# Kernel optimization log

Measured on AMD Instinct MI355X. Metric: run time of the kernel, lower is better.

The kernel has to match this reference:

```python
import jax, jax.numpy as jnp
import numpy as np

N_NODES = 100000
N_EDGES = 3200000
IN_SIZE, HIDDEN, OUT_SIZE = 512, 16, 64


def setup_inputs() -> dict:
    key = jax.random.key(0)
    k1, k2, k3, k4, k5, k6 = jax.random.split(key, 6)
    x = jax.random.normal(k1, (N_NODES, IN_SIZE), dtype=jnp.float32)
    src = jax.random.randint(k2, (N_EDGES,), 0, N_NODES, dtype=jnp.int64)
    dst = jax.random.randint(k3, (N_EDGES,), 0, N_NODES, dtype=jnp.int64)
    # Glorot-style init like dgl GraphConv
    W1 = jax.random.normal(k4, (IN_SIZE, HIDDEN), dtype=jnp.float32) * (1.0 / np.sqrt(IN_SIZE))
    b1 = jnp.zeros((HIDDEN,), dtype=jnp.float32)
    W2 = jax.random.normal(k5, (HIDDEN, OUT_SIZE), dtype=jnp.float32) * (1.0 / np.sqrt(HIDDEN))
    b2 = jnp.zeros((OUT_SIZE,), dtype=jnp.float32)
    return {"x": x, "W1": W1, "b1": b1, "W2": W2, "b2": b2, "src": src, "dst": dst}


def _degree_norms(src, dst, n_nodes):
    ones = jnp.ones(src.shape[0], dtype=jnp.float32)
    deg_out = jnp.clip(jax.ops.segment_sum(ones, src, num_segments=n_nodes), 1.0)
    deg_in = jnp.clip(jax.ops.segment_sum(ones, dst, num_segments=n_nodes), 1.0)
    return deg_out ** -0.5, deg_in ** -0.5  # norm='both' as in dgl GraphConv


def _graph_conv(x, W, b, src, dst, norm_src, norm_dst, transform_first):
    # dgl GraphConv: applies W before aggregation when in_feats > out_feats
    h = x * norm_src[:, None]
    if transform_first:
        h = h @ W
    # SpMM: gather from src, scatter-sum to dst
    agg = jax.ops.segment_sum(h[src], dst, num_segments=x.shape[0])
    if not transform_first:
        agg = agg @ W
    return agg * norm_dst[:, None] + b


def reference(x, W1, b1, W2, b2, src, dst):
    n = x.shape[0]
    norm_src, norm_dst = _degree_norms(src, dst, n)
    h = _graph_conv(x, W1, b1, src, dst, norm_src, norm_dst, transform_first=True)  # 512>16
    h = jax.nn.relu(h)
    out = _graph_conv(h, W2, b2, src, dst, norm_src, norm_dst, transform_first=False)  # 16<64
    return out
```

## Files before the change

kernel.cpp:

```cpp
#include <hip/hip_runtime.h>

#define NT 256
#define NBC 49
#define CAPC 69632
#define EPBC 8192
#define CAP 16384
#define MAXF 512

typedef __bf16 bf16x8 __attribute__((ext_vector_type(8)));
typedef float f32x4 __attribute__((ext_vector_type(4)));

__device__ __forceinline__ unsigned short f2bf(float f) {
    unsigned int u = __float_as_uint(f);
    unsigned int r = u + 0x7FFFu + ((u >> 16) & 1u);
    return (unsigned short)(r >> 16);
}
__device__ __forceinline__ float bf2f(unsigned short h) {
    return __uint_as_float(((unsigned int)h) << 16);
}

__global__ __launch_bounds__(512) void init_all(int* __restrict__ gcurCD,
                                                int* __restrict__ gcurCS,
                                                int* __restrict__ gcurF,
                                                const float* __restrict__ W1,
                                                unsigned short* __restrict__ w1t_hi,
                                                unsigned short* __restrict__ w1t_lo, int nbf) {
    if (blockIdx.x == 0) {
        int i = threadIdx.x;
        if (i < NBC) { gcurCD[i] = i * CAPC; gcurCS[i] = i * CAPC; }
        if (i < nbf) gcurF[i] = i * CAP;
    } else {
        int t = (blockIdx.x - 1) * 512 + threadIdx.x;
        if (t < 512 * 16) {
            int k = t >> 4, c = t & 15;
            float f = W1[k * 16 + c];
            unsigned short h = f2bf(f);
            w1t_hi[c * 512 + k] = h;
            w1t_lo[c * 512 + k] = f2bf(f - bf2f(h));
        }
    }
}

__global__ __launch_bounds__(NT) void coarse_scatter(const int* __restrict__ src,
                                                     const int* __restrict__ dst,
                                                     int* __restrict__ gcurCD,
                                                     int* __restrict__ gcurCS,
                                                     unsigned int* __restrict__ ebinCD,
                                                     unsigned short* __restrict__ ebinCS,
                                                     int e) {
    __shared__ int hD[NBC], hS[NBC], cD[NBC], cS[NBC];
    int tid = threadIdx.x;
    if (tid < NBC) { hD[tid] = 0; hS[tid] = 0; }
    __syncthreads();
    int p0 = blockIdx.x * EPBC;
    int pend = min(p0 + EPBC, e);
    for (int p = p0 + tid; p < pend; p += NT) {
        atomicAdd(&hD[dst[p] >> 11], 1);
        atomicAdd(&hS[src[p] >> 11], 1);
    }
    __syncthreads();
    if (tid < NBC) {
        cD[tid] = hD[tid] ? atomicAdd(&gcurCD[tid], hD[tid]) : 0;
        cS[tid] = hS[tid] ? atomicAdd(&gcurCS[tid], hS[tid]) : 0;
    }
    __syncthreads();
    for (int p = p0 + tid; p < pend; p += NT) {
        int s = src[p], d = dst[p];
        int c = d >> 11;
        int slot = atomicAdd(&cD[c], 1);
        if (slot < (c + 1) * CAPC)
            ebinCD[slot] = (unsigned int)s | ((unsigned int)(d & 2047) << 17);
        int cs = s >> 11;
        int slot2 = atomicAdd(&cS[cs], 1);
        if (slot2 < (cs + 1) * CAPC)
            ebinCS[slot2] = (unsigned short)(s & 2047);
    }
}

__global__ __launch_bounds__(NT) void fine_scatter(const unsigned int* __restrict__ ebinCD,
                                                   const int* __restrict__ gcurCD,
                                                   int* __restrict__ gcurF,
                                                   unsigned int* __restrict__ ebinD) {
    __shared__ int hF[8], cF[8];
    int c = blockIdx.x >> 3, k = blockIdx.x & 7;
    int tid = threadIdx.x;
    if (tid < 8) hF[tid] = 0;
    __syncthreads();
    int p0c = c * CAPC;
    int p1 = gcurCD[c];
    int len = p1 - p0c;
    int chunk = (len + 7) >> 3;
    int q0 = p0c + k * chunk;
    int q1 = min(q0 + chunk, p1);
    for (int p = q0 + tid; p < q1; p += NT)
        atomicAdd(&hF[(ebinCD[p] >> 25) & 7], 1);
    __syncthreads();
    if (tid < 8) {
        int h = hF[tid];
        cF[tid] = h ? atomicAdd(&gcurF[c * 8 + tid], h) : 0;
    }
    __syncthreads();
    for (int p = q0 + tid; p < q1; p += NT) {
        unsigned int w = ebinCD[p];
        int f = (w >> 25) & 7;
        int slot = atomicAdd(&cF[f], 1);
        if (slot < (c * 8 + f + 1) * CAP)
            ebinD[slot] = (w & 0x1FFFFu) | (((w >> 17) & 255u) << 17);
    }
}

__global__ __launch_bounds__(NT) void s_hist(const unsigned short* __restrict__ ebinCS,
                                             const int* __restrict__ gcurCS,
                                             int* __restrict__ cntS, int n) {
    __shared__ int cnt[2048];
    int c = blockIdx.x >> 3, k = blockIdx.x & 7;
    int tid = threadIdx.x;
    for (int i = tid; i < 2048; i += NT) cnt[i] = 0;
    __syncthreads();
    int p0c = c * CAPC;
    int p1 = gcurCS[c];
    int len = p1 - p0c;
    int chunk = (len + 7) >> 3;
    int q0 = p0c + k * chunk;
    int q1 = min(q0 + chunk, p1);
    for (int p = q0 + tid; p < q1; p += NT)
        atomicAdd(&cnt[ebinCS[p]], 1);
    __syncthreads();
    int node0 = c * 2048;
    for (int i = tid; i < 2048; i += NT) {
        int v = cnt[i];
        if (v && node0 + i < n) atomicAdd(&cntS[node0 + i], v);
    }
}

#define GR 64
__global__ __launch_bounds__(NT) void gemm1_mfma(const float* __restrict__ x,
                                                 const unsigned short* __restrict__ w1t_hi,
                                                 const unsigned short* __restrict__ w1t_lo,
                                                 const int* __restrict__ cntS,
                                                 unsigned short* __restrict__ y1bf, int n) {
    __shared__ __attribute__((aligned(16))) unsigned short sh_hi[GR][72];
    __shared__ __attribute__((aligned(16))) unsigned short sh_lo[GR][72];
    int tid = threadIdx.x;
    int w = tid >> 6, l = tid & 63;
    int row0 = blockIdx.x * GR;

    f32x4 acc = {0.f, 0.f, 0.f, 0.f};
    int col = l & 15;
    int kq = (l >> 4) * 8;
    int arow = w * 16 + (l & 15);

    for (int kc = 0; kc < 512; kc += 64) {
        __syncthreads();
#pragma unroll
        for (int i = 0; i < 4; i++) {
            int idx = tid + i * NT;
            int r = idx >> 4;
            int c4 = idx & 15;
            int grow = row0 + r;
            float4 v = make_float4(0.f, 0.f, 0.f, 0.f);
            if (grow < n) v = *(const float4*)&x[(size_t)grow * 512 + kc + c4 * 4];
            ushort4 hv, lv;
            hv.x = f2bf(v.x); lv.x = f2bf(v.x - bf2f(hv.x));
            hv.y = f2bf(v.y); lv.y = f2bf(v.y - bf2f(hv.y));
            hv.z = f2bf(v.z); lv.z = f2bf(v.z - bf2f(hv.z));
            hv.w = f2bf(v.w); lv.w = f2bf(v.w - bf2f(hv.w));
            *(ushort4*)&sh_hi[r][c4 * 4] = hv;
            *(ushort4*)&sh_lo[r][c4 * 4] = lv;
        }
        __syncthreads();
#pragma unroll
        for (int ks = 0; ks < 2; ks++) {
            int klocal = ks * 32 + kq;
            bf16x8 a_hi = *(const bf16x8*)&sh_hi[arow][klocal];
            bf16x8 a_lo = *(const bf16x8*)&sh_lo[arow][klocal];
            int kglob = kc + klocal;
            bf16x8 b_hi = *(const bf16x8*)&w1t_hi[col * 512 + kglob];
            bf16x8 b_lo = *(const bf16x8*)&w1t_lo[col * 512 + kglob];
            acc = __builtin_amdgcn_mfma_f32_16x16x32_bf16(a_hi, b_hi, acc, 0, 0, 0);
            acc = __builtin_amdgcn_mfma_f32_16x16x32_bf16(a_lo, b_hi, acc, 0, 0, 0);
            acc = __builtin_amdgcn_mfma_f32_16x16x32_bf16(a_hi, b_lo, acc, 0, 0, 0);
        }
    }

    int rbase = (l >> 4) * 4;
#pragma unroll
    for (int reg = 0; reg < 4; reg++) {
        int grow = row0 + w * 16 + rbase + reg;
        if (grow < n) {
            float ns = rsqrtf((float)max(cntS[grow], 1));
            y1bf[(size_t)grow * 16 + col] = f2bf(acc[reg] * ns);
        }
    }
}

__global__ __launch_bounds__(NT) void dst_fill(const unsigned int* __restrict__ ebinD,
                                               const int* __restrict__ gcurF,
                                               int* __restrict__ rowoff,
                                               int* __restrict__ rowend,
                                               float* __restrict__ norm_dst,
                                               int* __restrict__ esrc, int n) {
    __shared__ int cnt[256], cur[256], tmp[256];
    int b = blockIdx.x, tid = threadIdx.x;
    cnt[tid] = 0;
    __syncthreads();
    int p0 = b * CAP, p1 = gcurF[b];
    for (int p = p0 + tid; p < p1; p += NT) atomicAdd(&cnt[ebinD[p] >> 17], 1);
    __syncthreads();
    int v = cnt[tid];
    int val = v;
    tmp[tid] = val;
    __syncthreads();
    for (int off = 1; off < 256; off <<= 1) {
        int a = (tid >= off) ? tmp[tid - off] : 0;
        __syncthreads();
        val += a;
        tmp[tid] = val;
        __syncthreads();
    }
    int excl = val - v;
    int node = (b << 8) + tid;
    if (node < n) {
        rowoff[node] = p0 + excl;
        rowend[node] = p0 + excl + v;
        norm_dst[node] = rsqrtf((float)max(v, 1));
    }
    cur[tid] = p0 + excl;
    __syncthreads();
    for (int p = p0 + tid; p < p1; p += NT) {
        unsigned int w = ebinD[p];
        int pos = atomicAdd(&cur[w >> 17], 1);
        esrc[pos] = (int)(w & 0x1FFFFu);
    }
}

__global__ __launch_bounds__(NT) void aggregate_act(const unsigned short* __restrict__ feat,
                                                    const int* __restrict__ rowoff,
                                                    const int* __restrict__ rowend,
                                                    const int* __restrict__ esrc,
                                                    const float* __restrict__ norm_dst,
                                                    const int* __restrict__ cntS,
                                                    const float* __restrict__ b1,
                                                    unsigned short* __restrict__ h1s, int n) {
    int tid = threadIdx.x;
    int d = blockIdx.x * 16 + (tid >> 4);
    int j = tid & 15;
    if (d >= n) return;
    int p = rowoff[d], end = rowend[d];
    float a0 = 0.f, a1 = 0.f, a2 = 0.f, a3 = 0.f;
    for (; p + 3 < end; p += 4) {
        int s0 = esrc[p], s1 = esrc[p + 1], s2 = esrc[p + 2], s3 = esrc[p + 3];
        a0 += bf2f(feat[(size_t)s0 * 16 + j]);
        a1 += bf2f(feat[(size_t)s1 * 16 + j]);
        a2 += bf2f(feat[(size_t)s2 * 16 + j]);
        a3 += bf2f(feat[(size_t)s3 * 16 + j]);
    }
    for (; p < end; ++p) a0 += bf2f(feat[(size_t)esrc[p] * 16 + j]);
    float acc = (a0 + a1) + (a2 + a3);
    float ns = rsqrtf((float)max(cntS[d], 1));
    float v = fmaxf(acc * norm_dst[d] + b1[j], 0.f) * ns;
    h1s[(size_t)d * 16 + j] = f2bf(v);
}

__global__ __launch_bounds__(NT) void aggregate_final(const unsigned short* __restrict__ feat,
                                                      const int* __restrict__ rowoff,
                                                      const int* __restrict__ rowend,
                                                      const int* __restrict__ esrc,
                                                      const float* __restrict__ norm_dst,
                                                      const float* __restrict__ W2,
                                                      const float* __restrict__ b2,
                                                      float* __restrict__ out, int n) {
    __shared__ float sW[16 * 64];
    int tid = threadIdx.x;
    *(float4*)&sW[tid * 4] = *(const float4*)&W2[tid * 4];
    __syncthreads();
    int d = blockIdx.x * 16 + (tid >> 4);
    int j = tid & 15;
    if (d >= n) return;
    int p = rowoff[d], end = rowend[d];
    float a0 = 0.f, a1 = 0.f, a2 = 0.f, a3 = 0.f;
    for (; p + 3 < end; p += 4) {
        int s0 = esrc[p], s1 = esrc[p + 1], s2 = esrc[p + 2], s3 = esrc[p + 3];
        a0 += bf2f(feat[(size_t)s0 * 16 + j]);
        a1 += bf2f(feat[(size_t)s1 * 16 + j]);
        a2 += bf2f(feat[(size_t)s2 * 16 + j]);
        a3 += bf2f(feat[(size_t)s3 * 16 + j]);
    }
    for (; p < end; ++p) a0 += bf2f(feat[(size_t)esrc[p] * 16 + j]);
    float acc = (a0 + a1) + (a2 + a3);
    float nd = norm_dst[d];
    float o0 = 0.f, o1 = 0.f, o2 = 0.f, o3 = 0.f;
#pragma unroll
    for (int k = 0; k < 16; k++) {
        float ak = __shfl(acc, k, 16);
        o0 += ak * sW[k * 64 + j];
        o1 += ak * sW[k * 64 + j + 16];
        o2 += ak * sW[k * 64 + j + 32];
        o3 += ak * sW[k * 64 + j + 48];
    }
    size_t ob = (size_t)d * 64;
    out[ob + j]      = o0 * nd + b2[j];
    out[ob + j + 16] = o1 * nd + b2[j + 16];
    out[ob + j + 32] = o2 * nd + b2[j + 32];
    out[ob + j + 48] = o3 * nd + b2[j + 48];
}

extern "C" void kernel_launch(void* const* d_in, const int* in_sizes, int n_in,
                              void* d_out, int out_size, void* d_ws, size_t ws_size,
                              hipStream_t stream) {
    const float* x  = (const float*)d_in[0];
    const float* W1 = (const float*)d_in[1];
    const float* b1 = (const float*)d_in[2];
    const float* W2 = (const float*)d_in[3];
    const float* b2 = (const float*)d_in[4];
    const int* src  = (const int*)d_in[5];
    const int* dst  = (const int*)d_in[6];

    int n = in_sizes[0] / 512;
    int e = in_sizes[5];
    float* out = (float*)d_out;

    int nbf = (n + 255) >> 8;

    char* ws = (char*)d_ws;
    size_t off = 0;
    auto alloc = [&](size_t bytes) { size_t o = off; off = (off + bytes + 255) & ~(size_t)255; return o; };
    int*   cntS   = (int*)(ws + alloc((size_t)n * 4));
    size_t zero_end = off;
    int*   gcurCD = (int*)(ws + alloc(NBC * 4));
    int*   gcurCS = (int*)(ws + alloc(NBC * 4));
    int*   gcurF  = (int*)(ws + alloc(MAXF * 4));
    float* norm_dst = (float*)(ws + alloc((size_t)n * 4));
    int*   rowoff   = (int*)(ws + alloc((size_t)n * 4));
    int*   rowend   = (int*)(ws + alloc((size_t)n * 4));
    unsigned int*   ebinCD = (unsigned int*)(ws + alloc((size_t)NBC * CAPC * 4));
    unsigned short* ebinCS = (unsigned short*)(ws + alloc((size_t)NBC * CAPC * 2));
    unsigned int*   ebinD  = (unsigned int*)(ws + alloc((size_t)nbf * CAP * 4));
    int*   esrc  = (int*)(ws + alloc((size_t)nbf * CAP * 4));
    unsigned short* y1bf = (unsigned short*)(ws + alloc((size_t)n * 16 * 2));
    unsigned short* h1s  = (unsigned short*)(ws + alloc((size_t)n * 16 * 2));
    unsigned short* w1t_hi = (unsigned short*)(ws + alloc(16 * 512 * 2));
    unsigned short* w1t_lo = (unsigned short*)(ws + alloc(16 * 512 * 2));
    if (off > ws_size) return;

    int cbb = (e + EPBC - 1) / EPBC;
    int fbb = NBC * 8;
    int grb = (n + GR - 1) / GR;
    int agb = (n + 15) / 16;

    hipMemsetAsync(cntS, 0, zero_end, stream);

    init_all       <<<17, 512, 0, stream>>>(gcurCD, gcurCS, gcurF, W1, w1t_hi, w1t_lo, nbf);
    coarse_scatter <<<cbb, NT, 0, stream>>>(src, dst, gcurCD, gcurCS, ebinCD, ebinCS, e);
    fine_scatter   <<<fbb, NT, 0, stream>>>(ebinCD, gcurCD, gcurF, ebinD);
    s_hist         <<<fbb, NT, 0, stream>>>(ebinCS, gcurCS, cntS, n);
    gemm1_mfma     <<<grb, NT, 0, stream>>>(x, w1t_hi, w1t_lo, cntS, y1bf, n);
    dst_fill       <<<nbf, NT, 0, stream>>>(ebinD, gcurF, rowoff, rowend, norm_dst, esrc, n);
    aggregate_act  <<<agb, NT, 0, stream>>>(y1bf, rowoff, rowend, esrc, norm_dst, cntS, b1, h1s, n);
    aggregate_final<<<agb, NT, 0, stream>>>(h1s, rowoff, rowend, esrc, norm_dst, W2, b2, out, n);
}
```

Baseline: 245.0 us.

## Merge fine scatter with source histogram and use one wavefront per node in aggregation

Merges the fine_scatter and s_hist kernels into one launch whose blocks branch on block index, so the two independent passes run side by side and one launch is saved. The two aggregation kernels now give each destination node a full 64-lane wavefront instead of 16 lanes. Within a node, four lane groups walk the neighbour list in parallel, two edges per group per step, and the partial sums are combined with cross-lane shuffles. This exposes more memory-level parallelism on the irregular gathers. In exchange, many lanes sit idle on low-degree nodes, and there are four times as many blocks.

```diff
diff --git a/kernel.cpp b/kernel.cpp
--- a/kernel.cpp
+++ b/kernel.cpp
@@ -77,59 +77,60 @@
     }
 }
 
-__global__ __launch_bounds__(NT) void fine_scatter(const unsigned int* __restrict__ ebinCD,
-                                                   const int* __restrict__ gcurCD,
-                                                   int* __restrict__ gcurF,
-                                                   unsigned int* __restrict__ ebinD) {
-    __shared__ int hF[8], cF[8];
-    int c = blockIdx.x >> 3, k = blockIdx.x & 7;
+__global__ __launch_bounds__(NT) void fine_plus_shist(const unsigned int* __restrict__ ebinCD,
+                                                      const int* __restrict__ gcurCD,
+                                                      int* __restrict__ gcurF,
+                                                      unsigned int* __restrict__ ebinD,
+                                                      const unsigned short* __restrict__ ebinCS,
+                                                      const int* __restrict__ gcurCS,
+                                                      int* __restrict__ cntS, int n) {
     int tid = threadIdx.x;
-    if (tid < 8) hF[tid] = 0;
-    __syncthreads();
-    int p0c = c * CAPC;
-    int p1 = gcurCD[c];
-    int len = p1 - p0c;
-    int chunk = (len + 7) >> 3;
-    int q0 = p0c + k * chunk;
-    int q1 = min(q0 + chunk, p1);
-    for (int p = q0 + tid; p < q1; p += NT)
-        atomicAdd(&hF[(ebinCD[p] >> 25) & 7], 1);
-    __syncthreads();
-    if (tid < 8) {
-        int h = hF[tid];
-        cF[tid] = h ? atomicAdd(&gcurF[c * 8 + tid], h) : 0;
-    }
-    __syncthreads();
-    for (int p = q0 + tid; p < q1; p += NT) {
-        unsigned int w = ebinCD[p];
-        int f = (w >> 25) & 7;
-        int slot = atomicAdd(&cF[f], 1);
-        if (slot < (c * 8 + f + 1) * CAP)
-            ebinD[slot] = (w & 0x1FFFFu) | (((w >> 17) & 255u) << 17);
-    }
-}
-
-__global__ __launch_bounds__(NT) void s_hist(const unsigned short* __restrict__ ebinCS,
-                                             const int* __restrict__ gcurCS,
-                                             int* __restrict__ cntS, int n) {
-    __shared__ int cnt[2048];
-    int c = blockIdx.x >> 3, k = blockIdx.x & 7;
-    int tid = threadIdx.x;
-    for (int i = tid; i < 2048; i += NT) cnt[i] = 0;
-    __syncthreads();
-    int p0c = c * CAPC;
-    int p1 = gcurCS[c];
-    int len = p1 - p0c;
-    int chunk = (len + 7) >> 3;
-    int q0 = p0c + k * chunk;
-    int q1 = min(q0 + chunk, p1);
-    for (int p = q0 + tid; p < q1; p += NT)
-        atomicAdd(&cnt[ebinCS[p]], 1);
-    __syncthreads();
-    int node0 = c * 2048;
-    for (int i = tid; i < 2048; i += NT) {
-        int v = cnt[i];
-        if (v && node0 + i < n) atomicAdd(&cntS[node0 + i], v);
+    if (blockIdx.x < NBC * 8) {
+        __shared__ int hF[8], cF[8];
+        int c = blockIdx.x >> 3, k = blockIdx.x & 7;
+        if (tid < 8) hF[tid] = 0;
+        __syncthreads();
+        int p0c = c * CAPC;
+        int p1 = gcurCD[c];
+        int len = p1 - p0c;
+        int chunk = (len + 7) >> 3;
+        int q0 = p0c + k * chunk;
+        int q1 = min(q0 + chunk, p1);
+        for (int p = q0 + tid; p < q1; p += NT)
+            atomicAdd(&hF[(ebinCD[p] >> 25) & 7], 1);
+        __syncthreads();
+        if (tid < 8) {
+            int h = hF[tid];
+            cF[tid] = h ? atomicAdd(&gcurF[c * 8 + tid], h) : 0;
+        }
+        __syncthreads();
+        for (int p = q0 + tid; p < q1; p += NT) {
+            unsigned int w = ebinCD[p];
+            int f = (w >> 25) & 7;
+            int slot = atomicAdd(&cF[f], 1);
+            if (slot < (c * 8 + f + 1) * CAP)
+                ebinD[slot] = (w & 0x1FFFFu) | (((w >> 17) & 255u) << 17);
+        }
+    } else {
+        __shared__ int cnt[2048];
+        int bb = blockIdx.x - NBC * 8;
+        int c = bb >> 3, k = bb & 7;
+        for (int i = tid; i < 2048; i += NT) cnt[i] = 0;
+        __syncthreads();
+        int p0c = c * CAPC;
+        int p1 = gcurCS[c];
+        int len = p1 - p0c;
+        int chunk = (len + 7) >> 3;
+        int q0 = p0c + k * chunk;
+        int q1 = min(q0 + chunk, p1);
+        for (int p = q0 + tid; p < q1; p += NT)
+            atomicAdd(&cnt[ebinCS[p]], 1);
+        __syncthreads();
+        int node0 = c * 2048;
+        for (int i = tid; i < 2048; i += NT) {
+            int v = cnt[i];
+            if (v && node0 + i < n) atomicAdd(&cntS[node0 + i], v);
+        }
     }
 }
 
@@ -242,24 +243,26 @@
                                                     const int* __restrict__ cntS,
                                                     const float* __restrict__ b1,
                                                     unsigned short* __restrict__ h1s, int n) {
-    int tid = threadIdx.x;
-    int d = blockIdx.x * 16 + (tid >> 4);
-    int j = tid & 15;
+    int d = blockIdx.x * 4 + (threadIdx.x >> 6);
     if (d >= n) return;
-    int p = rowoff[d], end = rowend[d];
-    float a0 = 0.f, a1 = 0.f, a2 = 0.f, a3 = 0.f;
-    for (; p + 3 < end; p += 4) {
-        int s0 = esrc[p], s1 = esrc[p + 1], s2 = esrc[p + 2], s3 = esrc[p + 3];
-        a0 += bf2f(feat[(size_t)s0 * 16 + j]);
-        a1 += bf2f(feat[(size_t)s1 * 16 + j]);
-        a2 += bf2f(feat[(size_t)s2 * 16 + j]);
-        a3 += bf2f(feat[(size_t)s3 * 16 + j]);
-    }
-    for (; p < end; ++p) a0 += bf2f(feat[(size_t)esrc[p] * 16 + j]);
-    float acc = (a0 + a1) + (a2 + a3);
-    float ns = rsqrtf((float)max(cntS[d], 1));
-    float v = fmaxf(acc * norm_dst[d] + b1[j], 0.f) * ns;
-    h1s[(size_t)d * 16 + j] = f2bf(v);
+    int l = threadIdx.x & 63;
+    int g = l >> 4, j = l & 15;
+    int p0 = rowoff[d], p1 = rowend[d];
+    float acc = 0.f;
+    for (int p = p0; p < p1; p += 8) {
+        int pe0 = p + g, pe1 = p + 4 + g;
+        float v0 = 0.f, v1 = 0.f;
+        if (pe0 < p1) v0 = bf2f(feat[(size_t)esrc[pe0] * 16 + j]);
+        if (pe1 < p1) v1 = bf2f(feat[(size_t)esrc[pe1] * 16 + j]);
+        acc += v0 + v1;
+    }
+    acc += __shfl_xor(acc, 16);
+    acc += __shfl_xor(acc, 32);
+    if (l < 16) {
+        float ns = rsqrtf((float)max(cntS[d], 1));
+        float v = fmaxf(acc * norm_dst[d] + b1[j], 0.f) * ns;
+        h1s[(size_t)d * 16 + j] = f2bf(v);
+    }
 }
 
 __global__ __launch_bounds__(NT) void aggregate_final(const unsigned short* __restrict__ feat,
@@ -274,35 +277,29 @@
     int tid = threadIdx.x;
     *(float4*)&sW[tid * 4] = *(const float4*)&W2[tid * 4];
     __syncthreads();
-    int d = blockIdx.x * 16 + (tid >> 4);
-    int j = tid & 15;
+    int d = blockIdx.x * 4 + (tid >> 6);
     if (d >= n) return;
-    int p = rowoff[d], end = rowend[d];
-    float a0 = 0.f, a1 = 0.f, a2 = 0.f, a3 = 0.f;
-    for (; p + 3 < end; p += 4) {
-        int s0 = esrc[p], s1 = esrc[p + 1], s2 = esrc[p + 2], s3 = esrc[p + 3];
-        a0 += bf2f(feat[(size_t)s0 * 16 + j]);
-        a1 += bf2f(feat[(size_t)s1 * 16 + j]);
-        a2 += bf2f(feat[(size_t)s2 * 16 + j]);
-        a3 += bf2f(feat[(size_t)s3 * 16 + j]);
-    }
-    for (; p < end; ++p) a0 += bf2f(feat[(size_t)esrc[p] * 16 + j]);
-    float acc = (a0 + a1) + (a2 + a3);
+    int l = tid & 63;
+    int g = l >> 4, j = l & 15;
+    int p0 = rowoff[d], p1 = rowend[d];
+    float acc = 0.f;
+    for (int p = p0; p < p1; p += 8) {
+        int pe0 = p + g, pe1 = p + 4 + g;
+        float v0 = 0.f, v1 = 0.f;
+        if (pe0 < p1) v0 = bf2f(feat[(size_t)esrc[pe0] * 16 + j]);
+        if (pe1 < p1) v1 = bf2f(feat[(size_t)esrc[pe1] * 16 + j]);
+        acc += v0 + v1;
+    }
+    acc += __shfl_xor(acc, 16);
+    acc += __shfl_xor(acc, 32);
     float nd = norm_dst[d];
-    float o0 = 0.f, o1 = 0.f, o2 = 0.f, o3 = 0.f;
+    float o = 0.f;
 #pragma unroll
     for (int k = 0; k < 16; k++) {
         float ak = __shfl(acc, k, 16);
-        o0 += ak * sW[k * 64 + j];
-        o1 += ak * sW[k * 64 + j + 16];
-        o2 += ak * sW[k * 64 + j + 32];
-        o3 += ak * sW[k * 64 + j + 48];
-    }
-    size_t ob = (size_t)d * 64;
-    out[ob + j]      = o0 * nd + b2[j];
-    out[ob + j + 16] = o1 * nd + b2[j + 16];
-    out[ob + j + 32] = o2 * nd + b2[j + 32];
-    out[ob + j + 48] = o3 * nd + b2[j + 48];
+        o += ak * sW[k * 64 + l];
+    }
+    out[(size_t)d * 64 + l] = o * nd + b2[l];
 }
 
 extern "C" void kernel_launch(void* const* d_in, const int* in_sizes, int n_in,
@@ -344,16 +341,15 @@
     if (off > ws_size) return;
 
     int cbb = (e + EPBC - 1) / EPBC;
-    int fbb = NBC * 8;
+    int fsb = NBC * 16;
     int grb = (n + GR - 1) / GR;
-    int agb = (n + 15) / 16;
+    int agb = (n + 3) / 4;
 
     hipMemsetAsync(cntS, 0, zero_end, stream);
 
     init_all       <<<17, 512, 0, stream>>>(gcurCD, gcurCS, gcurF, W1, w1t_hi, w1t_lo, nbf);
     coarse_scatter <<<cbb, NT, 0, stream>>>(src, dst, gcurCD, gcurCS, ebinCD, ebinCS, e);
-    fine_scatter   <<<fbb, NT, 0, stream>>>(ebinCD, gcurCD, gcurF, ebinD);
-    s_hist         <<<fbb, NT, 0, stream>>>(ebinCS, gcurCS, cntS, n);
+    fine_plus_shist<<<fsb, NT, 0, stream>>>(ebinCD, gcurCD, gcurF, ebinD, ebinCS, gcurCS, cntS, n);
     gemm1_mfma     <<<grb, NT, 0, stream>>>(x, w1t_hi, w1t_lo, cntS, y1bf, n);
     dst_fill       <<<nbf, NT, 0, stream>>>(ebinD, gcurF, rowoff, rowend, norm_dst, esrc, n);
     aggregate_act  <<<agb, NT, 0, stream>>>(y1bf, rowoff, rowend, esrc, norm_dst, cntS, b1, h1s, n);
```

After: 311.7 us. 1.27x slower.
